# Performance work log

Measured on AMD Instinct MI355X. Metric: run time of the kernel, lower is better.

Reference implementation:

```python
import jax, jax.numpy as jnp
import numpy as np
import math

DIM = 1024
WINDOW = 16
NUM_HEADS = 16
HEAD_DIM = DIM // NUM_HEADS
SCALE = math.sqrt(HEAD_DIM)
LN_EPS = 1e-5


def _gather_window(z, W):
    # z: [B, T, H, C] -> [B, T, H, W, C]; nb[:, t, :, w, :] = z[:, t-1-w] (zeros if t-1-w < 0)
    B, T, H, C = z.shape
    t = jnp.arange(T)[:, None]
    w = jnp.arange(W)[None, :]
    idx = t - 1 - w                      # [T, W]
    valid = idx >= 0
    idxc = jnp.clip(idx, 0, T - 1)
    nb = z[:, idxc]                      # [B, T, W, H, C]
    nb = jnp.where(valid[None, :, :, None, None], nb, jnp.zeros((), z.dtype))
    return nb.transpose(0, 1, 3, 2, 4)   # [B, T, H, W, C]


def setup_inputs() -> dict:
    key = jax.random.key(0)
    k0, k1, k2, k3 = jax.random.split(key, 4)
    B, T, D = 2, 4096, DIM
    x = jax.random.normal(k0, (B, T, D), dtype=jnp.float32)
    wq = jax.random.normal(k1, (D, D), dtype=jnp.float32) * 0.02
    wkv = jax.random.normal(k2, (2 * D, D), dtype=jnp.float32) * 0.02  # torch Linear weight layout [out,in]
    wo = jax.random.normal(k3, (D, D), dtype=jnp.float32) * 0.02
    gamma = jnp.ones((D,), dtype=jnp.float32)
    beta = jnp.zeros((D,), dtype=jnp.float32)
    return {"x": x, "wq": wq, "wkv": wkv, "wo": wo, "gamma": gamma, "beta": beta}


def reference(x, wq, wkv, wo, gamma, beta):
    B, T, D = x.shape
    H, HD, W = NUM_HEADS, HEAD_DIM, WINDOW
    q = (x @ wq.T).reshape(B, T, H, HD)
    kv = (x @ wkv.T).reshape(B, T, H, 2 * HD)
    nb_kv = _gather_window(kv, W)                    # [B, T, H, W, 2*HD]
    nb_k, nb_v = nb_kv[..., :HD], nb_kv[..., HD:]
    tau = jax.nn.sigmoid(jnp.einsum('bthd,bthwd->bthw', q, nb_k) / SCALE)
    msg = jnp.einsum('bthw,bthwd->bthd', tau, nb_v)  # [B, T, H, HD]
    y = x + msg.reshape(B, T, D) @ wo.T
    mu = jnp.mean(y, axis=-1, keepdims=True)
    var = jnp.mean((y - mu) ** 2, axis=-1, keepdims=True)
    out = (y - mu) * jax.lax.rsqrt(var + LN_EPS) * gamma + beta
    return out
```

## Files before the change

kernel.cpp:

```cpp
#include <hip/hip_runtime.h>
#include <hip/hip_bf16.h>

#define D_MODEL 1024
#define SEQ_T   4096
#define NBATCH  2
#define NHEADS  16
#define HEAD_D  64
#define WIN     16

typedef __attribute__((ext_vector_type(8))) short bf16x8;
typedef __attribute__((ext_vector_type(8))) unsigned short u16x8;
typedef __attribute__((ext_vector_type(4))) float f32x4;

__device__ __forceinline__ unsigned short f2bf(float f) {
  union { float f; unsigned int u; } v; v.f = f;
  unsigned int r = v.u + 0x7fffu + ((v.u >> 16) & 1u);
  return (unsigned short)(r >> 16);
}
__device__ __forceinline__ float bf2f(unsigned short u) {
  union { unsigned int u; float f; } v; v.u = ((unsigned int)u) << 16;
  return v.f;
}

__global__ __launch_bounds__(256) void cast_f32_bf16(const float4* __restrict__ src,
                                                     ushort* __restrict__ dst, int n4) {
  int i = blockIdx.x * 256 + threadIdx.x;
  if (i >= n4) return;
  float4 v = src[i];
  ushort4 o;
  o.x = f2bf(v.x); o.y = f2bf(v.y); o.z = f2bf(v.z); o.w = f2bf(v.w);
  *(ushort4*)(dst + (size_t)i * 4) = o;
}

__global__ __launch_bounds__(256) void cast_weights(const float4* __restrict__ wq,
                                                    const float4* __restrict__ wkv,
                                                    const float4* __restrict__ wo,
                                                    ushort* __restrict__ dst) {
  int i = blockIdx.x * 256 + threadIdx.x;
  const float4* src;
  int off;
  if (i < 262144) { src = wq; off = 0; }
  else if (i < 786432) { src = wkv; off = 262144; }
  else { src = wo; off = 786432; }
  float4 v = src[i - off];
  ushort4 o;
  o.x = f2bf(v.x); o.y = f2bf(v.y); o.z = f2bf(v.z); o.w = f2bf(v.w);
  *(ushort4*)(dst + (size_t)i * 4) = o;
}

#define SBAR() __builtin_amdgcn_s_barrier()
#define LGKM0() asm volatile("s_waitcnt lgkmcnt(0)" ::: "memory")
#define VMC(n) asm volatile("s_waitcnt vmcnt(" #n ")" ::: "memory")

template <int EPI>
__global__ __launch_bounds__(512, 2) void gemm_8w(const ushort* __restrict__ A,
                                                  const ushort* __restrict__ Bt,
                                                  ushort* __restrict__ Cb,
                                                  float* __restrict__ Cf,
                                                  const float* __restrict__ resid,
                                                  int M, int N, int K) {
  extern __shared__ char smem[];
  const int NTK = K >> 6;
  const int tid = threadIdx.x;
  const int wid = tid >> 6;
  const int lane = tid & 63;
  const int m0 = blockIdx.y * 256;
  const int n0 = blockIdx.x * 128;

  const int l8 = lane >> 3;
  const int lchunk = (lane & 7) ^ (l8 & 7);
  const ushort* pA = A + (size_t)(m0 + wid * 8 + l8) * K + lchunk * 8;
  const ushort* pB = Bt + (size_t)(n0 + wid * 8 + l8) * K + lchunk * 8;

#define STAGE_A(kt, db)                                                                    \
  {                                                                                        \
    _Pragma("unroll") for (int j = 0; j < 4; ++j) {                                        \
      const ushort* gp = pA + (size_t)(j * 64) * K + (size_t)(kt) * 64;                    \
      char* lp = smem + (db) * 32768 + (j * 8 + wid) * 1024;                               \
      __builtin_amdgcn_global_load_lds((const __attribute__((address_space(1))) void*)gp,  \
                                       (__attribute__((address_space(3))) void*)lp, 16, 0, 0); \
    }                                                                                      \
  }
#define STAGE_B(kt, db)                                                                    \
  {                                                                                        \
    _Pragma("unroll") for (int j = 0; j < 2; ++j) {                                        \
      const ushort* gp = pB + (size_t)(j * 64) * K + (size_t)(kt) * 64;                    \
      char* lp = smem + 65536 + (db) * 16384 + (j * 8 + wid) * 1024;                       \
      __builtin_amdgcn_global_load_lds((const __attribute__((address_space(1))) void*)gp,  \
                                       (__attribute__((address_space(3))) void*)lp, 16, 0, 0); \
    }                                                                                      \
  }

  const int fr = lane & 15;
  const int g = lane >> 4;
  const int wr = wid >> 1;
  const int wc = wid & 1;
  int aRow[4], bRow[2][2], ch[2];
#pragma unroll
  for (int mi = 0; mi < 4; ++mi) aRow[mi] = (wr * 64 + mi * 16 + fr) * 128;
#pragma unroll
  for (int nq = 0; nq < 2; ++nq)
#pragma unroll
    for (int ni = 0; ni < 2; ++ni) bRow[nq][ni] = (wc * 64 + nq * 32 + ni * 16 + fr) * 128;
#pragma unroll
  for (int kk = 0; kk < 2; ++kk) ch[kk] = ((kk * 4 + g) ^ (fr & 7)) * 16;

  f32x4 acc[2][4][2];
#pragma unroll
  for (int nq = 0; nq < 2; ++nq)
#pragma unroll
    for (int mi = 0; mi < 4; ++mi)
#pragma unroll
      for (int ni = 0; ni < 2; ++ni) acc[nq][mi][ni] = (f32x4){0.f, 0.f, 0.f, 0.f};

  bf16x8 a[4][2], b0[2][2], b1[2][2];

  STAGE_A(0, 0); STAGE_B(0, 0); STAGE_A(1, 1);
  VMC(4);
  SBAR();

#define PHASE_MFMA(nq, bfr)                                                    \
  __builtin_amdgcn_s_setprio(1);                                               \
  _Pragma("unroll") for (int kk = 0; kk < 2; ++kk)                             \
    _Pragma("unroll") for (int mi = 0; mi < 4; ++mi)                           \
      _Pragma("unroll") for (int ni = 0; ni < 2; ++ni)                         \
        acc[nq][mi][ni] = __builtin_amdgcn_mfma_f32_16x16x32_bf16(             \
            a[mi][kk], bfr[ni][kk], acc[nq][mi][ni], 0, 0, 0);                 \
  __builtin_amdgcn_s_setprio(0);

#pragma unroll 1
  for (int t = 0; t < NTK; ++t) {
    const int db = t & 1;
    const int u1 = (t + 1 < NTK) ? t + 1 : NTK - 1;
    const int u2 = (t + 2 < NTK) ? t + 2 : NTK - 1;
    const int d1 = u1 & 1, d2 = u2 & 1;
    const char* Ab = smem + db * 32768;
    const char* Bb = smem + 65536 + db * 16384;

#pragma unroll
    for (int mi = 0; mi < 4; ++mi)
#pragma unroll
      for (int kk = 0; kk < 2; ++kk)
        a[mi][kk] = *(const bf16x8*)(Ab + aRow[mi] + ch[kk]);
#pragma unroll
    for (int ni = 0; ni < 2; ++ni)
#pragma unroll
      for (int kk = 0; kk < 2; ++kk)
        b0[ni][kk] = *(const bf16x8*)(Bb + bRow[0][ni] + ch[kk]);
    STAGE_B(u1, d1);
    LGKM0();
    PHASE_MFMA(0, b0);
    VMC(2);
    SBAR();

#pragma unroll
    for (int ni = 0; ni < 2; ++ni)
#pragma unroll
      for (int kk = 0; kk < 2; ++kk)
        b1[ni][kk] = *(const bf16x8*)(Bb + bRow[1][ni] + ch[kk]);
    STAGE_A(u2, d2);
    LGKM0();
    PHASE_MFMA(1, b1);
    VMC(4);
    SBAR();
  }

  const int cc = lane & 15;
  const int cr4 = (lane >> 4) * 4;
#pragma unroll
  for (int nq = 0; nq < 2; ++nq)
#pragma unroll
    for (int mi = 0; mi < 4; ++mi)
#pragma unroll
      for (int ni = 0; ni < 2; ++ni)
#pragma unroll
        for (int r = 0; r < 4; ++r) {
          int row = m0 + wr * 64 + mi * 16 + cr4 + r;
          int col = n0 + wc * 64 + nq * 32 + ni * 16 + cc;
          size_t idx = (size_t)row * N + col;
          float v = acc[nq][mi][ni][r];
          if (EPI == 0) {
            Cb[idx] = f2bf(v);
          } else {
            Cf[idx] = v + resid[idx];
          }
        }
#undef STAGE_A
#undef STAGE_B
#undef PHASE_MFMA
}

__global__ __launch_bounds__(256) void attn_win_mfma(const ushort* __restrict__ qkv,
                                                     ushort* __restrict__ msg) {
  __shared__ ushort Ks[80][72];
  __shared__ ushort Vt[64][88];
  __shared__ ushort Ps[4][16][40];

  const int tile = blockIdx.x;
  const int h = blockIdx.y;
  const int b = blockIdx.z;
  const int t0 = tile * 64;
  const size_t rowbase = (size_t)b * SEQ_T;
  const int tid = threadIdx.x;
  const int wave = tid >> 6;
  const int lane = tid & 63;

  for (int chunk = tid; chunk < 1280; chunk += 256) {
    int r = chunk >> 4;
    int c = (chunk & 15) * 8;
    int t = t0 - 16 + r;
    u16x8 u = {0, 0, 0, 0, 0, 0, 0, 0};
    if (t >= 0)
      u = *(const u16x8*)(qkv + (rowbase + t) * 3072 + 1024 + (size_t)h * 128 + c);
    if (c < 64) {
      *(u16x8*)&Ks[r][c] = u;
    } else {
      int d0 = c - 64;
#pragma unroll
      for (int j = 0; j < 8; ++j) Vt[d0 + j][r] = u[j];
    }
  }
  __syncthreads();

  const int fr = lane & 15;
  const int g = lane >> 4;
  const int rbase = wave * 16;

  bf16x8 qa[2];
#pragma unroll
  for (int kk = 0; kk < 2; ++kk)
    qa[kk] = *(const bf16x8*)(qkv + (rowbase + t0 + wave * 16 + fr) * 3072 +
                              (size_t)h * 64 + kk * 32 + g * 8);

  f32x4 sacc[2];
  sacc[0] = (f32x4){0.f, 0.f, 0.f, 0.f};
  sacc[1] = (f32x4){0.f, 0.f, 0.f, 0.f};
#pragma unroll
  for (int kk = 0; kk < 2; ++kk) {
#pragma unroll
    for (int nt = 0; nt < 2; ++nt) {
      bf16x8 kb = *(const bf16x8*)&Ks[rbase + nt * 16 + fr][kk * 32 + g * 8];
      sacc[nt] = __builtin_amdgcn_mfma_f32_16x16x32_bf16(qa[kk], kb, sacc[nt], 0, 0, 0);
    }
  }

#pragma unroll
  for (int nt = 0; nt < 2; ++nt) {
    int tk = t0 - 16 + rbase + nt * 16 + fr;
#pragma unroll
    for (int reg = 0; reg < 4; ++reg) {
      int t = t0 + wave * 16 + g * 4 + reg;
      float tau = 0.f;
      if (tk >= 0 && tk >= t - WIN && tk <= t - 1)
        tau = 1.f / (1.f + __expf(-sacc[nt][reg] * 0.125f));
      Ps[wave][g * 4 + reg][nt * 16 + fr] = f2bf(tau);
    }
  }
  __syncthreads();

  bf16x8 pa = *(const bf16x8*)&Ps[wave][fr][g * 8];
#pragma unroll
  for (int ct = 0; ct < 4; ++ct) {
    bf16x8 vb = *(const bf16x8*)&Vt[ct * 16 + fr][rbase + g * 8];
    f32x4 m = __builtin_amdgcn_mfma_f32_16x16x32_bf16(pa, vb, (f32x4){0.f, 0.f, 0.f, 0.f}, 0, 0, 0);
#pragma unroll
    for (int reg = 0; reg < 4; ++reg) {
      int t = t0 + wave * 16 + g * 4 + reg;
      msg[(rowbase + t) * 1024 + (size_t)h * 64 + ct * 16 + fr] = f2bf(m[reg]);
    }
  }
}

__global__ __launch_bounds__(256) void layernorm_inplace(float* __restrict__ y,
                                                         const float* __restrict__ gamma,
                                                         const float* __restrict__ beta) {
  const int row = blockIdx.x;
  float* p = y + (size_t)row * D_MODEL;
  const int tid = threadIdx.x;
  float4 v = *(const float4*)&p[tid * 4];
  float s = v.x + v.y + v.z + v.w;
  float s2 = v.x * v.x + v.y * v.y + v.z * v.z + v.w * v.w;
#pragma unroll
  for (int m = 1; m < 64; m <<= 1) {
    s += __shfl_xor(s, m);
    s2 += __shfl_xor(s2, m);
  }
  __shared__ float red[8];
  const int wave = tid >> 6, lane = tid & 63;
  if (lane == 0) { red[wave] = s; red[4 + wave] = s2; }
  __syncthreads();
  s = red[0] + red[1] + red[2] + red[3];
  s2 = red[4] + red[5] + red[6] + red[7];
  const float mu = s * (1.f / D_MODEL);
  const float var = s2 * (1.f / D_MODEL) - mu * mu;
  const float rstd = rsqrtf(var + 1e-5f);
  float4 g = *(const float4*)&gamma[tid * 4];
  float4 be = *(const float4*)&beta[tid * 4];
  float4 o;
  o.x = (v.x - mu) * rstd * g.x + be.x;
  o.y = (v.y - mu) * rstd * g.y + be.y;
  o.z = (v.z - mu) * rstd * g.z + be.z;
  o.w = (v.w - mu) * rstd * g.w + be.w;
  *(float4*)&p[tid * 4] = o;
}

extern "C" void kernel_launch(void* const* d_in, const int* in_sizes, int n_in,
                              void* d_out, int out_size, void* d_ws, size_t ws_size,
                              hipStream_t stream) {
  (void)in_sizes; (void)n_in; (void)out_size; (void)ws_size;
  const float* x = (const float*)d_in[0];
  const float* wq = (const float*)d_in[1];
  const float* wkv = (const float*)d_in[2];
  const float* wo = (const float*)d_in[3];
  const float* gamma = (const float*)d_in[4];
  const float* beta = (const float*)d_in[5];
  float* out = (float*)d_out;

  ushort* xb = (ushort*)d_ws;
  ushort* wb = xb + (size_t)8192 * 1024;
  ushort* qkvb = wb + (size_t)4096 * 1024;
  ushort* msgb = qkvb + (size_t)8192 * 3072;

  const int M = NBATCH * SEQ_T;

  (void)hipFuncSetAttribute(reinterpret_cast<const void*>(&gemm_8w<0>),
                            hipFuncAttributeMaxDynamicSharedMemorySize, 98304);
  (void)hipFuncSetAttribute(reinterpret_cast<const void*>(&gemm_8w<1>),
                            hipFuncAttributeMaxDynamicSharedMemorySize, 98304);

  cast_f32_bf16<<<(M * D_MODEL / 4 + 255) / 256, 256, 0, stream>>>((const float4*)x, xb, M * D_MODEL / 4);
  cast_weights<<<4096, 256, 0, stream>>>((const float4*)wq, (const float4*)wkv,
                                         (const float4*)wo, wb);

  gemm_8w<0><<<dim3(3072 / 128, M / 256), 512, 98304, stream>>>(xb, wb, qkvb, nullptr, nullptr,
                                                                M, 3072, 1024);

  attn_win_mfma<<<dim3(SEQ_T / 64, NHEADS, NBATCH), 256, 0, stream>>>(qkvb, msgb);

  gemm_8w<1><<<dim3(1024 / 128, M / 256), 512, 98304, stream>>>(msgb, wb + (size_t)3072 * 1024,
                                                                nullptr, out, x, M, 1024, 1024);

  layernorm_inplace<<<M, 256, 0, stream>>>(out, gamma, beta);
}
```

Before: 135.5 us.

## Use a 256x192 tile GEMM for the QKV projection

Adds a dedicated bf16 MFMA GEMM kernel for the QKV projection. It uses a 256x192 output tile, up from 256x128, with double-buffered direct-to-LDS loads and interleaved staging of the A and B tiles. The wider tile raises operand reuse per loaded K-slab and cuts the grid from 768 to 512 blocks, which should reduce wave-quantization tail on the CUs. The costs are 112KB of LDS per block, more accumulator registers, and scalar bf16 stores in the epilogue.

Result: no change. 133.1 us (-1.8%).

```diff
diff --git a/kernel.cpp b/kernel.cpp
--- a/kernel.cpp
+++ b/kernel.cpp
@@ -21,6 +21,10 @@
   union { unsigned int u; float f; } v; v.u = ((unsigned int)u) << 16;
   return v.f;
 }
+
+#define SBAR() __builtin_amdgcn_s_barrier()
+#define LGKM0() asm volatile("s_waitcnt lgkmcnt(0)" ::: "memory")
+#define VMC(n) asm volatile("s_waitcnt vmcnt(" #n ")" ::: "memory")
 
 __global__ __launch_bounds__(256) void cast_f32_bf16(const float4* __restrict__ src,
                                                      ushort* __restrict__ dst, int n4) {
@@ -48,9 +52,151 @@
   *(ushort4*)(dst + (size_t)i * 4) = o;
 }
 
-#define SBAR() __builtin_amdgcn_s_barrier()
-#define LGKM0() asm volatile("s_waitcnt lgkmcnt(0)" ::: "memory")
-#define VMC(n) asm volatile("s_waitcnt vmcnt(" #n ")" ::: "memory")
+__global__ __launch_bounds__(512, 2) void gemm1_192(const ushort* __restrict__ A,
+                                                    const ushort* __restrict__ Bt,
+                                                    ushort* __restrict__ C,
+                                                    int M, int N, int K) {
+  extern __shared__ char smem[];
+  const int NTK = K >> 6;
+  const int tid = threadIdx.x;
+  const int wid = tid >> 6;
+  const int lane = tid & 63;
+  const int m0 = blockIdx.y * 256;
+  const int n0 = blockIdx.x * 192;
+
+  const int l8 = lane >> 3;
+  const int lchunk = (lane & 7) ^ (l8 & 7);
+  const ushort* pA = A + (size_t)(m0 + wid * 8 + l8) * K + lchunk * 8;
+  const ushort* pB = Bt + (size_t)(n0 + wid * 8 + l8) * K + lchunk * 8;
+
+#define STAGE_A(kt, db)                                                                    \
+  {                                                                                        \
+    _Pragma("unroll") for (int j = 0; j < 4; ++j) {                                        \
+      const ushort* gp = pA + (size_t)(j * 64) * K + (size_t)(kt) * 64;                    \
+      char* lp = smem + (db) * 32768 + (j * 8 + wid) * 1024;                               \
+      __builtin_amdgcn_global_load_lds((const __attribute__((address_space(1))) void*)gp,  \
+                                       (__attribute__((address_space(3))) void*)lp, 16, 0, 0); \
+    }                                                                                      \
+  }
+#define STAGE_B(kt, db)                                                                    \
+  {                                                                                        \
+    _Pragma("unroll") for (int j = 0; j < 3; ++j) {                                        \
+      const ushort* gp = pB + (size_t)(j * 64) * K + (size_t)(kt) * 64;                    \
+      char* lp = smem + 65536 + (db) * 24576 + (j * 8 + wid) * 1024;                       \
+      __builtin_amdgcn_global_load_lds((const __attribute__((address_space(1))) void*)gp,  \
+                                       (__attribute__((address_space(3))) void*)lp, 16, 0, 0); \
+    }                                                                                      \
+  }
+
+  const int fr = lane & 15;
+  const int g = lane >> 4;
+  const int wr = wid >> 1;
+  const int wc = wid & 1;
+  int aRow[4], bRow[6], ch[2];
+#pragma unroll
+  for (int mi = 0; mi < 4; ++mi) aRow[mi] = (wr * 64 + mi * 16 + fr) * 128;
+#pragma unroll
+  for (int j = 0; j < 6; ++j) bRow[j] = (wc * 96 + j * 16 + fr) * 128;
+#pragma unroll
+  for (int kk = 0; kk < 2; ++kk) ch[kk] = ((kk * 4 + g) ^ (fr & 7)) * 16;
+
+  f32x4 acc[4][6];
+#pragma unroll
+  for (int mi = 0; mi < 4; ++mi)
+#pragma unroll
+    for (int j = 0; j < 6; ++j) acc[mi][j] = (f32x4){0.f, 0.f, 0.f, 0.f};
+
+  bf16x8 a[4][2], b[3];
+
+  STAGE_A(0, 0); STAGE_B(0, 0); STAGE_A(1, 1);
+  VMC(4);
+  SBAR();
+
+#pragma unroll 1
+  for (int t = 0; t < NTK; ++t) {
+    const int db = t & 1;
+    const int u1 = (t + 1 < NTK) ? t + 1 : NTK - 1;
+    const int u2 = (t + 2 < NTK) ? t + 2 : NTK - 1;
+    const int d1 = u1 & 1, d2 = u2 & 1;
+    const char* Ab = smem + db * 32768;
+    const char* Bb = smem + 65536 + db * 24576;
+
+#pragma unroll
+    for (int mi = 0; mi < 4; ++mi)
+#pragma unroll
+      for (int kk = 0; kk < 2; ++kk)
+        a[mi][kk] = *(const bf16x8*)(Ab + aRow[mi] + ch[kk]);
+#pragma unroll
+    for (int ni = 0; ni < 3; ++ni) b[ni] = *(const bf16x8*)(Bb + bRow[ni] + ch[0]);
+    STAGE_B(u1, d1);
+    SBAR();
+    LGKM0();
+    __builtin_amdgcn_s_setprio(1);
+#pragma unroll
+    for (int mi = 0; mi < 4; ++mi)
+#pragma unroll
+      for (int ni = 0; ni < 3; ++ni)
+        acc[mi][ni] = __builtin_amdgcn_mfma_f32_16x16x32_bf16(a[mi][0], b[ni], acc[mi][ni], 0, 0, 0);
+    __builtin_amdgcn_s_setprio(0);
+    SBAR();
+
+#pragma unroll
+    for (int ni = 0; ni < 3; ++ni) b[ni] = *(const bf16x8*)(Bb + bRow[ni] + ch[1]);
+    STAGE_A(u2, d2);
+    SBAR();
+    LGKM0();
+    __builtin_amdgcn_s_setprio(1);
+#pragma unroll
+    for (int mi = 0; mi < 4; ++mi)
+#pragma unroll
+      for (int ni = 0; ni < 3; ++ni)
+        acc[mi][ni] = __builtin_amdgcn_mfma_f32_16x16x32_bf16(a[mi][1], b[ni], acc[mi][ni], 0, 0, 0);
+    __builtin_amdgcn_s_setprio(0);
+    SBAR();
+
+#pragma unroll
+    for (int ni = 0; ni < 3; ++ni) b[ni] = *(const bf16x8*)(Bb + bRow[3 + ni] + ch[0]);
+    SBAR();
+    LGKM0();
+    __builtin_amdgcn_s_setprio(1);
+#pragma unroll
+    for (int mi = 0; mi < 4; ++mi)
+#pragma unroll
+      for (int ni = 0; ni < 3; ++ni)
+        acc[mi][3 + ni] = __builtin_amdgcn_mfma_f32_16x16x32_bf16(a[mi][0], b[ni], acc[mi][3 + ni], 0, 0, 0);
+    __builtin_amdgcn_s_setprio(0);
+    SBAR();
+
+#pragma unroll
+    for (int ni = 0; ni < 3; ++ni) b[ni] = *(const bf16x8*)(Bb + bRow[3 + ni] + ch[1]);
+    SBAR();
+    LGKM0();
+    __builtin_amdgcn_s_setprio(1);
+#pragma unroll
+    for (int mi = 0; mi < 4; ++mi)
+#pragma unroll
+      for (int ni = 0; ni < 3; ++ni)
+        acc[mi][3 + ni] = __builtin_amdgcn_mfma_f32_16x16x32_bf16(a[mi][1], b[ni], acc[mi][3 + ni], 0, 0, 0);
+    __builtin_amdgcn_s_setprio(0);
+    VMC(4);
+    SBAR();
+  }
+
+  const int cc = lane & 15;
+  const int cr4 = (lane >> 4) * 4;
+#pragma unroll
+  for (int mi = 0; mi < 4; ++mi)
+#pragma unroll
+    for (int j = 0; j < 6; ++j)
+#pragma unroll
+      for (int r = 0; r < 4; ++r) {
+        int row = m0 + wr * 64 + mi * 16 + cr4 + r;
+        int col = n0 + wc * 96 + j * 16 + cc;
+        C[(size_t)row * N + col] = f2bf(acc[mi][j][r]);
+      }
+#undef STAGE_A
+#undef STAGE_B
+}
 
 template <int EPI>
 __global__ __launch_bounds__(512, 2) void gemm_8w(const ushort* __restrict__ A,
@@ -323,8 +469,8 @@
 
   const int M = NBATCH * SEQ_T;
 
-  (void)hipFuncSetAttribute(reinterpret_cast<const void*>(&gemm_8w<0>),
-                            hipFuncAttributeMaxDynamicSharedMemorySize, 98304);
+  (void)hipFuncSetAttribute(reinterpret_cast<const void*>(&gemm1_192),
+                            hipFuncAttributeMaxDynamicSharedMemorySize, 114688);
   (void)hipFuncSetAttribute(reinterpret_cast<const void*>(&gemm_8w<1>),
                             hipFuncAttributeMaxDynamicSharedMemorySize, 98304);
 
@@ -332,8 +478,7 @@
   cast_weights<<<4096, 256, 0, stream>>>((const float4*)wq, (const float4*)wkv,
                                          (const float4*)wo, wb);
 
-  gemm_8w<0><<<dim3(3072 / 128, M / 256), 512, 98304, stream>>>(xb, wb, qkvb, nullptr, nullptr,
-                                                                M, 3072, 1024);
+  gemm1_192<<<dim3(3072 / 192, M / 256), 512, 114688, stream>>>(xb, wb, qkvb, M, 3072, 1024);
 
   attn_win_mfma<<<dim3(SEQ_T / 64, NHEADS, NBATCH), 256, 0, stream>>>(qkvb, msgb);
 
```
